# Kernel tuning notes

Measured on AMD Instinct MI355X. Metric: run time of the kernel, lower is better.

Reference implementation:

```python
import jax, jax.numpy as jnp
import numpy as np

N = 200000       # nodes
E = 6400000      # edges (avg degree 32)
F_IN = 256       # num_features
HID = 16         # hardcoded hidden dim in GCN.__init__
C = 40           # num_classes


def setup_inputs() -> dict:
    key = jax.random.key(0)
    ks = jax.random.split(key, 8)
    x = jax.random.normal(ks[0], (N, F_IN), dtype=jnp.float32)
    edge_index = jax.random.randint(ks[1], (2, E), 0, N, dtype=jnp.int64)
    edge_weight = jax.random.uniform(ks[2], (E,), dtype=jnp.float32)
    # GCNConv params: glorot-ish linear weights + zero bias
    W1 = (jax.random.normal(ks[3], (F_IN, HID), dtype=jnp.float32) / np.float32(np.sqrt(F_IN)))
    b1 = jnp.zeros((HID,), jnp.float32)
    W2 = (jax.random.normal(ks[4], (HID, C), dtype=jnp.float32) / np.float32(np.sqrt(HID)))
    b2 = jnp.zeros((C,), jnp.float32)
    return {"x": x, "edge_index": edge_index, "edge_weight": edge_weight,
            "W1": W1, "b1": b1, "W2": W2, "b2": b2}


def _gcn_norm(edge_index, edge_weight, n):
    # PyG gcn_norm: add self-loops with weight 1, symmetric D^-1/2 A D^-1/2
    loops = jnp.arange(n, dtype=edge_index.dtype)
    src = jnp.concatenate([edge_index[0], loops])
    dst = jnp.concatenate([edge_index[1], loops])
    w = jnp.concatenate([edge_weight, jnp.ones((n,), edge_weight.dtype)])
    deg = jax.ops.segment_sum(w, dst, num_segments=n)
    dinv = jnp.where(deg > 0, jax.lax.rsqrt(deg), 0.0)  # inf -> 0 as in PyG
    return src, dst, dinv[src] * w * dinv[dst]


def reference(x, edge_index, edge_weight, W1, b1, W2, b2):
    n = x.shape[0]
    src, dst, norm = _gcn_norm(edge_index, edge_weight, n)

    def conv(h, W, b):
        h = h @ W                              # [N, out] transform first (PyG order)
        msg = h[src] * norm[:, None]           # gather + scale
        return jax.ops.segment_sum(msg, dst, num_segments=n) + b

    h = jax.nn.relu(conv(x, W1, b1))
    # F.dropout with training=False (eval) is identity; omitted for determinism
    return conv(h, W2, b2)
```

## Files before the change

### kernel.cpp

```cpp
#include <hip/hip_runtime.h>
#include <hip/hip_fp16.h>

#define NN 200000
#define NE 6400000
#define FIN 256
#define HID 16
#define NC 40
#define NBKT 782
#define NCHUNK 2048
#define EPC 3125
#define CPT 8
#define STAGE_CAP 9472

__global__ __launch_bounds__(256) void k_chist(const int* __restrict__ dst,
                                               int* __restrict__ hist_g) {
    __shared__ int sh[NBKT];
    int c = blockIdx.x;
    for (int j = threadIdx.x; j < NBKT; j += 256) sh[j] = 0;
    __syncthreads();
    int beg = c * EPC;
    for (int e = beg + threadIdx.x; e < beg + EPC; e += 256)
        atomicAdd(&sh[dst[e] >> 8], 1);
    __syncthreads();
    for (int j = threadIdx.x; j < NBKT; j += 256)
        hist_g[c * NBKT + j] = sh[j];
}

__global__ __launch_bounds__(256) void k_btotal(const int* __restrict__ hist_g,
                                                int* __restrict__ totals) {
    __shared__ int sm[256];
    int b = blockIdx.x, t = threadIdx.x;
    int s = 0;
#pragma unroll
    for (int j = 0; j < CPT; ++j)
        s += hist_g[(t * CPT + j) * NBKT + b];
    sm[t] = s;
    __syncthreads();
    for (int off = 128; off > 0; off >>= 1) {
        if (t < off) sm[t] += sm[t + off];
        __syncthreads();
    }
    if (t == 0) totals[b] = sm[0];
}

__global__ __launch_bounds__(1024) void k_bscan(const int* __restrict__ totals,
                                                int* __restrict__ binBase) {
    __shared__ int sm[1024];
    int t = threadIdx.x;
    int v = (t < NBKT) ? totals[t] : 0;
    sm[t] = v;
    __syncthreads();
    for (int off = 1; off < 1024; off <<= 1) {
        int x = (t >= off) ? sm[t - off] : 0;
        __syncthreads();
        sm[t] += x;
        __syncthreads();
    }
    if (t < NBKT) binBase[t] = sm[t] - v;
    if (t == 0) binBase[NBKT] = NE;
}

__global__ __launch_bounds__(256) void k_cscan(int* __restrict__ hist_g,
                                               const int* __restrict__ binBase) {
    __shared__ int sm[256];
    int b = blockIdx.x, t = threadIdx.x;
    int loc[CPT];
    int s = 0;
#pragma unroll
    for (int j = 0; j < CPT; ++j) {
        loc[j] = hist_g[(t * CPT + j) * NBKT + b];
        s += loc[j];
    }
    sm[t] = s;
    __syncthreads();
    for (int off = 1; off < 256; off <<= 1) {
        int x = (t >= off) ? sm[t - off] : 0;
        __syncthreads();
        sm[t] += x;
        __syncthreads();
    }
    int base = binBase[b] + sm[t] - s;
#pragma unroll
    for (int j = 0; j < CPT; ++j) {
        hist_g[(t * CPT + j) * NBKT + b] = base;
        base += loc[j];
    }
}

__global__ __launch_bounds__(256) void k_cscatter(const int* __restrict__ src,
                                                  const int* __restrict__ dst,
                                                  const float* __restrict__ w,
                                                  const int* __restrict__ coff,
                                                  int2* __restrict__ ebuf) {
    __shared__ int2 srec[EPC];
    __shared__ int sbase[NBKT];
    __shared__ int scur[NBKT];
    __shared__ int sgb[NBKT];
    __shared__ int sm[256];
    int c = blockIdx.x, t = threadIdx.x;
    for (int j = t; j < NBKT; j += 256) sbase[j] = 0;
    __syncthreads();
    int beg = c * EPC;
    for (int e = beg + t; e < beg + EPC; e += 256)
        atomicAdd(&sbase[dst[e] >> 8], 1);
    __syncthreads();
    int l[4];
    int s = 0;
#pragma unroll
    for (int q = 0; q < 4; ++q) {
        int j = t * 4 + q;
        l[q] = (j < NBKT) ? sbase[j] : 0;
        s += l[q];
    }
    sm[t] = s;
    __syncthreads();
    for (int off = 1; off < 256; off <<= 1) {
        int x = (t >= off) ? sm[t - off] : 0;
        __syncthreads();
        sm[t] += x;
        __syncthreads();
    }
    int base = sm[t] - s;
#pragma unroll
    for (int q = 0; q < 4; ++q) {
        int j = t * 4 + q;
        if (j < NBKT) {
            sbase[j] = base;
            scur[j]  = base;
            sgb[j]   = coff[c * NBKT + j] - base;
        }
        base += l[q];
    }
    __syncthreads();
    for (int e = beg + t; e < beg + EPC; e += 256) {
        int d = dst[e];
        int k = atomicAdd(&scur[d >> 8], 1);
        srec[k] = make_int2(src[e] | ((d & 255) << 18), __float_as_int(w[e]));
    }
    __syncthreads();
    for (int k = t; k < EPC; k += 256) {
        int lo = 0, hi = NBKT;
        while (hi - lo > 1) {
            int mid = (lo + hi) >> 1;
            if (sbase[mid] <= k) lo = mid; else hi = mid;
        }
        ebuf[sgb[lo] + k] = srec[k];
    }
}

__global__ __launch_bounds__(256) void k_bucket(const int* __restrict__ binBase,
                                                const int2* __restrict__ ebuf,
                                                float* __restrict__ dinv,
                                                int* __restrict__ row_start) {
    __shared__ int scnt[256];
    __shared__ float sdeg[256];
    __shared__ int ssc[256];
    int b = blockIdx.x, t = threadIdx.x;
    scnt[t] = 0;
    sdeg[t] = 1.0f;
    __syncthreads();
    int beg = binBase[b], end = binBase[b + 1];
    for (int e = beg + t; e < end; e += 256) {
        int2 r = ebuf[e];
        int dl = (r.x >> 18) & 255;
        atomicAdd(&scnt[dl], 1);
        atomicAdd(&sdeg[dl], __int_as_float(r.y));
    }
    __syncthreads();
    int node = b * 256 + t;
    if (node < NN) dinv[node] = rsqrtf(sdeg[t]);
    int v = scnt[t];
    ssc[t] = v;
    __syncthreads();
    for (int off = 1; off < 256; off <<= 1) {
        int x = (t >= off) ? ssc[t - off] : 0;
        __syncthreads();
        ssc[t] += x;
        __syncthreads();
    }
    if (node < NN) row_start[node] = beg + ssc[t] - v;
    if (b == NBKT - 1 && t == 0) row_start[NN] = NE;
}

__global__ __launch_bounds__(256) void k_bscatter(const int* __restrict__ binBase,
                                                  const int* __restrict__ row_start,
                                                  int2* __restrict__ ebuf) {
    __shared__ int2 srec[STAGE_CAP];
    __shared__ int scur[256];
    int b = blockIdx.x, t = threadIdx.x;
    int beg = binBase[b], end = binBase[b + 1];
    int cnt = end - beg;
    int node = b * 256 + t;
    scur[t] = (node < NN) ? (row_start[node] - beg) : 0;
    __syncthreads();
    for (int j = t; j < cnt; j += 256) {
        int2 r = ebuf[beg + j];
        int dl = (r.x >> 18) & 255;
        int k = atomicAdd(&scur[dl], 1);
        srec[k] = r;
    }
    __syncthreads();
    for (int j = t; j < cnt; j += 256)
        ebuf[beg + j] = srec[j];
}

__global__ __launch_bounds__(256) void k_gemm1(const float* __restrict__ x,
                                               const float* __restrict__ W1,
                                               const float* __restrict__ dinv,
                                               __half2* __restrict__ hp) {
    int row = blockIdx.x * 256 + threadIdx.x;
    if (row >= NN) return;
    float acc[HID];
#pragma unroll
    for (int f = 0; f < HID; ++f) acc[f] = 0.0f;
    const float4* x4 = reinterpret_cast<const float4*>(x + (size_t)row * FIN);
    for (int kk = 0; kk < FIN / 4; kk += 4) {
        float4 v0 = x4[kk], v1 = x4[kk + 1], v2 = x4[kk + 2], v3 = x4[kk + 3];
        float xs[16] = { v0.x, v0.y, v0.z, v0.w, v1.x, v1.y, v1.z, v1.w,
                         v2.x, v2.y, v2.z, v2.w, v3.x, v3.y, v3.z, v3.w };
        int kbase = kk * 4;
#pragma unroll
        for (int j = 0; j < 16; ++j) {
            int k = kbase + j;
#pragma unroll
            for (int f = 0; f < HID; ++f)
                acc[f] = fmaf(xs[j], W1[k * HID + f], acc[f]);
        }
    }
    float di = dinv[row];
    __half2 o[8];
#pragma unroll
    for (int j = 0; j < 8; ++j)
        o[j] = __floats2half2_rn(acc[2*j] * di, acc[2*j+1] * di);
    float4* st = reinterpret_cast<float4*>(hp + (size_t)row * 8);
    st[0] = *reinterpret_cast<float4*>(&o[0]);
    st[1] = *reinterpret_cast<float4*>(&o[4]);
}

__device__ __forceinline__ void fma_row16(const float4 u0, const float4 u1, float nv,
                                          float4& a0, float4& a1, float4& a2, float4& a3) {
    const __half2* ha = reinterpret_cast<const __half2*>(&u0);
    const __half2* hb = reinterpret_cast<const __half2*>(&u1);
    float2 f;
    f = __half22float2(ha[0]); a0.x = fmaf(f.x, nv, a0.x); a0.y = fmaf(f.y, nv, a0.y);
    f = __half22float2(ha[1]); a0.z = fmaf(f.x, nv, a0.z); a0.w = fmaf(f.y, nv, a0.w);
    f = __half22float2(ha[2]); a1.x = fmaf(f.x, nv, a1.x); a1.y = fmaf(f.y, nv, a1.y);
    f = __half22float2(ha[3]); a1.z = fmaf(f.x, nv, a1.z); a1.w = fmaf(f.y, nv, a1.w);
    f = __half22float2(hb[0]); a2.x = fmaf(f.x, nv, a2.x); a2.y = fmaf(f.y, nv, a2.y);
    f = __half22float2(hb[1]); a2.z = fmaf(f.x, nv, a2.z); a2.w = fmaf(f.y, nv, a2.w);
    f = __half22float2(hb[2]); a3.x = fmaf(f.x, nv, a3.x); a3.y = fmaf(f.y, nv, a3.y);
    f = __half22float2(hb[3]); a3.z = fmaf(f.x, nv, a3.z); a3.w = fmaf(f.y, nv, a3.w);
}

union H2F2 { __half2 h[2]; float2 f; };

__global__ __launch_bounds__(256) void k_gather1(const int* __restrict__ row_start,
                                                 const int2* __restrict__ edges,
                                                 const __half2* __restrict__ hp,
                                                 const float* __restrict__ dinv,
                                                 const float* __restrict__ b1,
                                                 __half2* __restrict__ h1p) {
    int t = blockIdx.x * 256 + threadIdx.x;
    int i = t >> 2;
    int sub = t & 3;
    int beg = row_start[i];
    int end = row_start[i + 1];
    float4 a0 = make_float4(0.f,0.f,0.f,0.f), a1 = a0, a2 = a0, a3 = a0;
    if (sub == 0) {
        const float4* r4 = reinterpret_cast<const float4*>(hp + (size_t)i * 8);
        fma_row16(r4[0], r4[1], 1.0f, a0, a1, a2, a3);
    }
    int p = beg + sub;
    for (; p + 4 < end; p += 8) {
        int2 ea = edges[p];
        int2 eb = edges[p + 4];
        const float4* ra = reinterpret_cast<const float4*>(hp + (size_t)(ea.x & 0x3FFFF) * 8);
        const float4* rb = reinterpret_cast<const float4*>(hp + (size_t)(eb.x & 0x3FFFF) * 8);
        float4 u0 = ra[0], u1 = ra[1], v0 = rb[0], v1 = rb[1];
        fma_row16(u0, u1, __int_as_float(ea.y), a0, a1, a2, a3);
        fma_row16(v0, v1, __int_as_float(eb.y), a0, a1, a2, a3);
    }
    if (p < end) {
        int2 ev = edges[p];
        const float4* r4 = reinterpret_cast<const float4*>(hp + (size_t)(ev.x & 0x3FFFF) * 8);
        fma_row16(r4[0], r4[1], __int_as_float(ev.y), a0, a1, a2, a3);
    }
#pragma unroll
    for (int m = 1; m <= 2; m <<= 1) {
        a0.x += __shfl_xor(a0.x, m); a0.y += __shfl_xor(a0.y, m);
        a0.z += __shfl_xor(a0.z, m); a0.w += __shfl_xor(a0.w, m);
        a1.x += __shfl_xor(a1.x, m); a1.y += __shfl_xor(a1.y, m);
        a1.z += __shfl_xor(a1.z, m); a1.w += __shfl_xor(a1.w, m);
        a2.x += __shfl_xor(a2.x, m); a2.y += __shfl_xor(a2.y, m);
        a2.z += __shfl_xor(a2.z, m); a2.w += __shfl_xor(a2.w, m);
        a3.x += __shfl_xor(a3.x, m); a3.y += __shfl_xor(a3.y, m);
        a3.z += __shfl_xor(a3.z, m); a3.w += __shfl_xor(a3.w, m);
    }
    float4 q = (sub == 0) ? a0 : (sub == 1) ? a1 : (sub == 2) ? a2 : a3;
    float di = dinv[i];
    float4 bb = reinterpret_cast<const float4*>(b1)[sub];
    q.x = di * fmaxf(fmaf(di, q.x, bb.x), 0.f);
    q.y = di * fmaxf(fmaf(di, q.y, bb.y), 0.f);
    q.z = di * fmaxf(fmaf(di, q.z, bb.z), 0.f);
    q.w = di * fmaxf(fmaf(di, q.w, bb.w), 0.f);
    H2F2 pk;
    pk.h[0] = __floats2half2_rn(q.x, q.y);
    pk.h[1] = __floats2half2_rn(q.z, q.w);
    reinterpret_cast<float2*>(h1p + (size_t)i * 8)[sub] = pk.f;
}

__global__ __launch_bounds__(256) void k_gather2(const int* __restrict__ row_start,
                                                 const int2* __restrict__ edges,
                                                 const __half2* __restrict__ h1p,
                                                 const float* __restrict__ dinv,
                                                 const float* __restrict__ W2,
                                                 const float* __restrict__ b2,
                                                 float* __restrict__ out) {
    __shared__ float sW2[HID * NC];
    __shared__ float sb2[NC];
    {
        int tt = threadIdx.x;
        for (int j = tt; j < HID * NC; j += 256) sW2[j] = W2[j];
        if (tt < NC) sb2[tt] = b2[tt];
    }
    __syncthreads();
    int t = blockIdx.x * 256 + threadIdx.x;
    int i = t >> 2;
    int sub = t & 3;
    int beg = row_start[i];
    int end = row_start[i + 1];
    float4 a0 = make_float4(0.f,0.f,0.f,0.f), a1 = a0, a2 = a0, a3 = a0;
    if (sub == 0) {
        const float4* r4 = reinterpret_cast<const float4*>(h1p + (size_t)i * 8);
        fma_row16(r4[0], r4[1], 1.0f, a0, a1, a2, a3);
    }
    int p = beg + sub;
    for (; p + 4 < end; p += 8) {
        int2 ea = edges[p];
        int2 eb = edges[p + 4];
        const float4* ra = reinterpret_cast<const float4*>(h1p + (size_t)(ea.x & 0x3FFFF) * 8);
        const float4* rb = reinterpret_cast<const float4*>(h1p + (size_t)(eb.x & 0x3FFFF) * 8);
        float4 u0 = ra[0], u1 = ra[1], v0 = rb[0], v1 = rb[1];
        fma_row16(u0, u1, __int_as_float(ea.y), a0, a1, a2, a3);
        fma_row16(v0, v1, __int_as_float(eb.y), a0, a1, a2, a3);
    }
    if (p < end) {
        int2 ev = edges[p];
        const float4* r4 = reinterpret_cast<const float4*>(h1p + (size_t)(ev.x & 0x3FFFF) * 8);
        fma_row16(r4[0], r4[1], __int_as_float(ev.y), a0, a1, a2, a3);
    }
#pragma unroll
    for (int m = 1; m <= 2; m <<= 1) {
        a0.x += __shfl_xor(a0.x, m); a0.y += __shfl_xor(a0.y, m);
        a0.z += __shfl_xor(a0.z, m); a0.w += __shfl_xor(a0.w, m);
        a1.x += __shfl_xor(a1.x, m); a1.y += __shfl_xor(a1.y, m);
        a1.z += __shfl_xor(a1.z, m); a1.w += __shfl_xor(a1.w, m);
        a2.x += __shfl_xor(a2.x, m); a2.y += __shfl_xor(a2.y, m);
        a2.z += __shfl_xor(a2.z, m); a2.w += __shfl_xor(a2.w, m);
        a3.x += __shfl_xor(a3.x, m); a3.y += __shfl_xor(a3.y, m);
        a3.z += __shfl_xor(a3.z, m); a3.w += __shfl_xor(a3.w, m);
    }
    float di = dinv[i];
    float av[HID] = { a0.x, a0.y, a0.z, a0.w, a1.x, a1.y, a1.z, a1.w,
                      a2.x, a2.y, a2.z, a2.w, a3.x, a3.y, a3.z, a3.w };
#pragma unroll
    for (int k = 0; k < HID; ++k) av[k] *= di;
    float* op = out + (size_t)i * NC + sub * 10;
#pragma unroll
    for (int c = 0; c < 10; ++c) {
        int col = sub * 10 + c;
        float s = sb2[col];
#pragma unroll
        for (int k = 0; k < HID; ++k)
            s = fmaf(av[k], sW2[k * NC + col], s);
        op[c] = s;
    }
}

extern "C" void kernel_launch(void* const* d_in, const int* in_sizes, int n_in,
                              void* d_out, int out_size, void* d_ws, size_t ws_size,
                              hipStream_t stream) {
    const float* x  = (const float*)d_in[0];
    const int*   ei = (const int*)d_in[1];
    const float* w  = (const float*)d_in[2];
    const float* W1 = (const float*)d_in[3];
    const float* b1 = (const float*)d_in[4];
    const float* W2 = (const float*)d_in[5];
    const float* b2 = (const float*)d_in[6];
    float* out = (float*)d_out;

    const int* src = ei;
    const int* dst = ei + NE;

    char* wsb = (char*)d_ws;
    float*   dinv      = (float*)  (wsb);
    int*     row_start = (int*)    (wsb + 200064LL * 4);
    int*     totals    = (int*)    (wsb + 400128LL * 4);
    int*     binBase   = (int*)    (wsb + 401152LL * 4);
    int2*    ebuf      = (int2*)   (wsb + 402176LL * 4);
    __half2* hp        = (__half2*)(wsb + 13202176LL * 4);
    int*     hist_g    = (int*)    (wsb + 13202176LL * 4);
    __half2* h1p       = (__half2*)(wsb + 14803776LL * 4);

    const int BN = (NN + 255) / 256;
    const int BG = (4 * NN) / 256;

    k_chist   <<<NCHUNK, 256, 0, stream>>>(dst, hist_g);
    k_btotal  <<<NBKT, 256, 0, stream>>>(hist_g, totals);
    k_bscan   <<<1, 1024, 0, stream>>>(totals, binBase);
    k_cscan   <<<NBKT, 256, 0, stream>>>(hist_g, binBase);
    k_cscatter<<<NCHUNK, 256, 0, stream>>>(src, dst, w, hist_g, ebuf);
    k_bucket  <<<NBKT, 256, 0, stream>>>(binBase, ebuf, dinv, row_start);
    k_bscatter<<<NBKT, 256, 0, stream>>>(binBase, row_start, ebuf);
    k_gemm1   <<<BN, 256, 0, stream>>>(x, W1, dinv, hp);
    k_gather1 <<<BG, 256, 0, stream>>>(row_start, ebuf, hp, dinv, b1, h1p);
    k_gather2 <<<BG, 256, 0, stream>>>(row_start, ebuf, h1p, dinv, W2, b2, out);
}
```

Before: 432.3 us.

## Merge scatter chunks, replace bucket binary search, deepen gather unrolling

Each k_cscatter block now handles two consecutive edge chunks, with half as many blocks. Each staged record keeps its bucket id in a small LDS array, so the per-record binary search over bucket bases at write-out is replaced by a direct lookup. The merge relies on the per-chunk offsets of adjacent chunks being contiguous within each bucket. Both neighbour-gather kernels now issue four independent edge/row loads per iteration instead of two, to keep more memory requests in flight. The cost is more LDS per scatter block (lower occupancy) and more registers in the gathers.

```diff
diff --git a/kernel.cpp b/kernel.cpp
--- a/kernel.cpp
+++ b/kernel.cpp
@@ -10,6 +10,9 @@
 #define NCHUNK 2048
 #define EPC 3125
 #define CPT 8
+#define SC_CHUNKS 2
+#define SC_EDGES (SC_CHUNKS * EPC)
+#define SC_BLOCKS (NCHUNK / SC_CHUNKS)
 #define STAGE_CAP 9472
 
 __global__ __launch_bounds__(256) void k_chist(const int* __restrict__ dst,
@@ -92,16 +95,18 @@
                                                   const float* __restrict__ w,
                                                   const int* __restrict__ coff,
                                                   int2* __restrict__ ebuf) {
-    __shared__ int2 srec[EPC];
+    __shared__ int2 srec[SC_EDGES];
+    __shared__ unsigned short sbkt[SC_EDGES];
     __shared__ int sbase[NBKT];
     __shared__ int scur[NBKT];
     __shared__ int sgb[NBKT];
     __shared__ int sm[256];
     int c = blockIdx.x, t = threadIdx.x;
+    int mc0 = c * SC_CHUNKS;
     for (int j = t; j < NBKT; j += 256) sbase[j] = 0;
     __syncthreads();
-    int beg = c * EPC;
-    for (int e = beg + t; e < beg + EPC; e += 256)
+    int beg = mc0 * EPC;
+    for (int e = beg + t; e < beg + SC_EDGES; e += 256)
         atomicAdd(&sbase[dst[e] >> 8], 1);
     __syncthreads();
     int l[4];
@@ -127,25 +132,21 @@
         if (j < NBKT) {
             sbase[j] = base;
             scur[j]  = base;
-            sgb[j]   = coff[c * NBKT + j] - base;
+            sgb[j]   = coff[mc0 * NBKT + j] - base;
         }
         base += l[q];
     }
     __syncthreads();
-    for (int e = beg + t; e < beg + EPC; e += 256) {
+    for (int e = beg + t; e < beg + SC_EDGES; e += 256) {
         int d = dst[e];
-        int k = atomicAdd(&scur[d >> 8], 1);
+        int b = d >> 8;
+        int k = atomicAdd(&scur[b], 1);
         srec[k] = make_int2(src[e] | ((d & 255) << 18), __float_as_int(w[e]));
-    }
-    __syncthreads();
-    for (int k = t; k < EPC; k += 256) {
-        int lo = 0, hi = NBKT;
-        while (hi - lo > 1) {
-            int mid = (lo + hi) >> 1;
-            if (sbase[mid] <= k) lo = mid; else hi = mid;
-        }
-        ebuf[sgb[lo] + k] = srec[k];
-    }
+        sbkt[k] = (unsigned short)b;
+    }
+    __syncthreads();
+    for (int k = t; k < SC_EDGES; k += 256)
+        ebuf[sgb[sbkt[k]] + k] = srec[k];
 }
 
 __global__ __launch_bounds__(256) void k_bucket(const int* __restrict__ binBase,
@@ -271,16 +272,22 @@
         fma_row16(r4[0], r4[1], 1.0f, a0, a1, a2, a3);
     }
     int p = beg + sub;
-    for (; p + 4 < end; p += 8) {
-        int2 ea = edges[p];
-        int2 eb = edges[p + 4];
-        const float4* ra = reinterpret_cast<const float4*>(hp + (size_t)(ea.x & 0x3FFFF) * 8);
-        const float4* rb = reinterpret_cast<const float4*>(hp + (size_t)(eb.x & 0x3FFFF) * 8);
-        float4 u0 = ra[0], u1 = ra[1], v0 = rb[0], v1 = rb[1];
-        fma_row16(u0, u1, __int_as_float(ea.y), a0, a1, a2, a3);
-        fma_row16(v0, v1, __int_as_float(eb.y), a0, a1, a2, a3);
-    }
-    if (p < end) {
+    for (; p + 12 < end; p += 16) {
+        int2 e0 = edges[p], e1 = edges[p + 4], e2 = edges[p + 8], e3 = edges[p + 12];
+        const float4* r0 = reinterpret_cast<const float4*>(hp + (size_t)(e0.x & 0x3FFFF) * 8);
+        const float4* r1 = reinterpret_cast<const float4*>(hp + (size_t)(e1.x & 0x3FFFF) * 8);
+        const float4* r2 = reinterpret_cast<const float4*>(hp + (size_t)(e2.x & 0x3FFFF) * 8);
+        const float4* r3 = reinterpret_cast<const float4*>(hp + (size_t)(e3.x & 0x3FFFF) * 8);
+        float4 u0a = r0[0], u0b = r0[1];
+        float4 u1a = r1[0], u1b = r1[1];
+        float4 u2a = r2[0], u2b = r2[1];
+        float4 u3a = r3[0], u3b = r3[1];
+        fma_row16(u0a, u0b, __int_as_float(e0.y), a0, a1, a2, a3);
+        fma_row16(u1a, u1b, __int_as_float(e1.y), a0, a1, a2, a3);
+        fma_row16(u2a, u2b, __int_as_float(e2.y), a0, a1, a2, a3);
+        fma_row16(u3a, u3b, __int_as_float(e3.y), a0, a1, a2, a3);
+    }
+    for (; p < end; p += 4) {
         int2 ev = edges[p];
         const float4* r4 = reinterpret_cast<const float4*>(hp + (size_t)(ev.x & 0x3FFFF) * 8);
         fma_row16(r4[0], r4[1], __int_as_float(ev.y), a0, a1, a2, a3);
@@ -335,16 +342,22 @@
         fma_row16(r4[0], r4[1], 1.0f, a0, a1, a2, a3);
     }
     int p = beg + sub;
-    for (; p + 4 < end; p += 8) {
-        int2 ea = edges[p];
-        int2 eb = edges[p + 4];
-        const float4* ra = reinterpret_cast<const float4*>(h1p + (size_t)(ea.x & 0x3FFFF) * 8);
-        const float4* rb = reinterpret_cast<const float4*>(h1p + (size_t)(eb.x & 0x3FFFF) * 8);
-        float4 u0 = ra[0], u1 = ra[1], v0 = rb[0], v1 = rb[1];
-        fma_row16(u0, u1, __int_as_float(ea.y), a0, a1, a2, a3);
-        fma_row16(v0, v1, __int_as_float(eb.y), a0, a1, a2, a3);
-    }
-    if (p < end) {
+    for (; p + 12 < end; p += 16) {
+        int2 e0 = edges[p], e1 = edges[p + 4], e2 = edges[p + 8], e3 = edges[p + 12];
+        const float4* r0 = reinterpret_cast<const float4*>(h1p + (size_t)(e0.x & 0x3FFFF) * 8);
+        const float4* r1 = reinterpret_cast<const float4*>(h1p + (size_t)(e1.x & 0x3FFFF) * 8);
+        const float4* r2 = reinterpret_cast<const float4*>(h1p + (size_t)(e2.x & 0x3FFFF) * 8);
+        const float4* r3 = reinterpret_cast<const float4*>(h1p + (size_t)(e3.x & 0x3FFFF) * 8);
+        float4 u0a = r0[0], u0b = r0[1];
+        float4 u1a = r1[0], u1b = r1[1];
+        float4 u2a = r2[0], u2b = r2[1];
+        float4 u3a = r3[0], u3b = r3[1];
+        fma_row16(u0a, u0b, __int_as_float(e0.y), a0, a1, a2, a3);
+        fma_row16(u1a, u1b, __int_as_float(e1.y), a0, a1, a2, a3);
+        fma_row16(u2a, u2b, __int_as_float(e2.y), a0, a1, a2, a3);
+        fma_row16(u3a, u3b, __int_as_float(e3.y), a0, a1, a2, a3);
+    }
+    for (; p < end; p += 4) {
         int2 ev = edges[p];
         const float4* r4 = reinterpret_cast<const float4*>(h1p + (size_t)(ev.x & 0x3FFFF) * 8);
         fma_row16(r4[0], r4[1], __int_as_float(ev.y), a0, a1, a2, a3);
@@ -409,7 +422,7 @@
     k_btotal  <<<NBKT, 256, 0, stream>>>(hist_g, totals);
     k_bscan   <<<1, 1024, 0, stream>>>(totals, binBase);
     k_cscan   <<<NBKT, 256, 0, stream>>>(hist_g, binBase);
-    k_cscatter<<<NCHUNK, 256, 0, stream>>>(src, dst, w, hist_g, ebuf);
+    k_cscatter<<<SC_BLOCKS, 256, 0, stream>>>(src, dst, w, hist_g, ebuf);
     k_bucket  <<<NBKT, 256, 0, stream>>>(binBase, ebuf, dinv, row_start);
     k_bscatter<<<NBKT, 256, 0, stream>>>(binBase, row_start, ebuf);
     k_gemm1   <<<BN, 256, 0, stream>>>(x, W1, dinv, hp);
```

Result: slower. 454.6 us (+5.2%).
